# Kernel tuning notes

Hardware: AMD Instinct MI355X
Metric: run time of the kernel (lower is better)

Reference implementation:

```python
import jax, jax.numpy as jnp
import numpy as np

B, C, H, W = 32, 512, 32, 32


def setup_inputs() -> dict:
    key = jax.random.key(0)
    ks = jax.random.split(key, 7)
    c2 = C // 2
    s_in = (1.0 / C) ** 0.5   # torch Conv2d default init scale (kernel 1x1)
    s_c2 = (1.0 / c2) ** 0.5
    return {
        "x": jax.random.normal(ks[0], (B, C, H, W), jnp.float32),
        "Wk": jax.random.normal(ks[1], (c2, C), jnp.float32) * s_in,
        "bk": jax.random.normal(ks[2], (c2,), jnp.float32) * s_in,
        "Wv": jax.random.normal(ks[3], (c2, C), jnp.float32) * s_in,
        "bv": jax.random.normal(ks[4], (c2,), jnp.float32) * s_in,
        "Wo": jax.random.normal(ks[5], (C, c2), jnp.float32) * s_c2,
        "bo": jax.random.normal(ks[6], (C,), jnp.float32) * s_c2,
    }


def reference(x, Wk, bk, Wv, bv, Wo, bo):
    Bn, Cn, Hn, Wn = x.shape
    c2 = Cn // 2
    M = Hn * Wn
    # 1x1 convs as channel contractions
    k = jnp.einsum('oc,bchw->bohw', Wk, x) + bk[None, :, None, None]   # [B,c2,H,W]
    v = jnp.einsum('oc,bchw->bohw', Wv, x) + bv[None, :, None, None]   # [B,c2,H,W]
    # torch .reshape(B, M, c2) reinterprets memory (NOT a transpose) -> same in jnp
    v = v.reshape(Bn, M, c2)                                           # [B,M,c2]
    kf = k.reshape(Bn, c2, M)                                          # [B,c2,M]
    # cov_feature: k^T I_hat k with I_hat = (1/M)I - (1/M^2)11^T
    #            = (1/M) k^T k - (1/M^2) s s^T,  s = sum over channels
    gram = jnp.einsum('bcm,bcn->bmn', kf, kf) / M                      # [B,M,M]
    s = kf.sum(axis=1)                                                 # [B,M]
    cov = gram - (s[:, :, None] * s[:, None, :]) / (M * M)
    attn = jax.nn.softmax(cov * (c2 ** -0.5), axis=-1)                 # [B,M,M]
    out = jnp.einsum('bmn,bnc->bmc', attn, v)                          # [B,M,c2]
    # torch .view(B, c2, H, W) is also a raw memory reinterpretation
    out = out.reshape(Bn, c2, Hn, Wn)
    out = jnp.einsum('oc,bchw->bohw', Wo, out) + bo[None, :, None, None]
    return out + x
```

## Files before the change

### kernel.cpp

```cpp
#include <hip/hip_runtime.h>


typedef short bf8 __attribute__((ext_vector_type(8)));
typedef float f32x4 __attribute__((ext_vector_type(4)));

#define MFMA16(a, b, c) __builtin_amdgcn_mfma_f32_16x16x32_bf16((a), (b), (c), 0, 0, 0)

__device__ __forceinline__ short f2bf(float x) {
  unsigned u = __float_as_uint(x);
  u += 0x7fffu + ((u >> 16) & 1u);
  return (short)(u >> 16);
}

__device__ __forceinline__ void gll16(const short* g, void* l) {
  __builtin_amdgcn_global_load_lds(
      (const __attribute__((address_space(1))) unsigned int*)g,
      (__attribute__((address_space(3))) unsigned int*)l, 16, 0, 0);
}

__device__ __forceinline__ void lgkm0() {
  asm volatile("s_waitcnt lgkmcnt(0)" ::: "memory");
}
template <int N>
__device__ __forceinline__ void waitv() {
  static_assert(N == 0 || N == 4 || N == 8, "bad vmcnt");
  if constexpr (N == 0) asm volatile("s_waitcnt vmcnt(0)" ::: "memory");
  else if constexpr (N == 4) asm volatile("s_waitcnt vmcnt(4)" ::: "memory");
  else asm volatile("s_waitcnt vmcnt(8)" ::: "memory");
}
__device__ __forceinline__ void barrier_relaxed() {
  asm volatile("" ::: "memory");
  __builtin_amdgcn_s_barrier();
  asm volatile("" ::: "memory");
}

__device__ __forceinline__ void gemm_core(const short* __restrict__ A,
                                          const short* __restrict__ B,
                                          int ldA, int ldB, int ksteps,
                                          char* smem, f32x4 acc[4][4]) {
  const int tid = threadIdx.x;
  const int w = tid >> 6, l = tid & 63;
  const int q = l >> 4, i = l & 15;
  const int wm = w & 1, wn = w >> 1;
  const int srow = l >> 3;
  const int gcol = ((l & 7) ^ srow) * 8;
  f32x4 zz = {0.f, 0.f, 0.f, 0.f};
  #pragma unroll
  for (int mt = 0; mt < 4; ++mt)
    #pragma unroll
    for (int nt = 0; nt < 4; ++nt) acc[mt][nt] = zz;

  for (int ks = 0; ks < ksteps; ++ks) {
    __syncthreads();
    const short* Ak = A + ks * 64 + gcol;
    const short* Bk = B + ks * 64 + gcol;
    #pragma unroll
    for (int j = 0; j < 4; ++j) {
      int s = w * 4 + j;
      size_t row = (size_t)(s * 8 + srow);
      gll16(Ak + row * ldA, smem + s * 1024);
      gll16(Bk + row * ldB, smem + 16384 + s * 1024);
    }
    __syncthreads();
    #pragma unroll
    for (int kq = 0; kq < 2; ++kq) {
      int sw = ((kq * 4 + q) ^ (i & 7)) * 16;
      bf8 af[4], bq[4];
      #pragma unroll
      for (int mt = 0; mt < 4; ++mt)
        af[mt] = *(const bf8*)(smem + (wm * 64 + mt * 16 + i) * 128 + sw);
      #pragma unroll
      for (int nt = 0; nt < 4; ++nt)
        bq[nt] = *(const bf8*)(smem + 16384 + (wn * 64 + nt * 16 + i) * 128 + sw);
      #pragma unroll
      for (int mt = 0; mt < 4; ++mt)
        #pragma unroll
        for (int nt = 0; nt < 4; ++nt)
          acc[mt][nt] = MFMA16(af[mt], bq[nt], acc[mt][nt]);
    }
  }
}

__global__ __launch_bounds__(256) void p0_xpose(const float* __restrict__ x,
                                                short* __restrict__ xT) {
  __shared__ float lds[64][65];
  int cb = blockIdx.x, sb = blockIdx.y, b = blockIdx.z;
  int t = threadIdx.x;
  int c0 = cb * 64, sp0 = sb * 64;
  const float4* x4 = reinterpret_cast<const float4*>(x);
  #pragma unroll
  for (int j = 0; j < 4; ++j) {
    int lin = t + 256 * j;
    int cl = lin >> 4, s4 = lin & 15;
    float4 v = x4[(((size_t)b * 512 + c0 + cl) * 1024 + sp0 + s4 * 4) >> 2];
    lds[cl][s4 * 4 + 0] = v.x; lds[cl][s4 * 4 + 1] = v.y;
    lds[cl][s4 * 4 + 2] = v.z; lds[cl][s4 * 4 + 3] = v.w;
  }
  __syncthreads();
  int spl = t >> 2, cs = (t & 3) * 16;
  bf8 o0, o1;
  #pragma unroll
  for (int j = 0; j < 8; ++j) o0[j] = f2bf(lds[cs + j][spl]);
  #pragma unroll
  for (int j = 0; j < 8; ++j) o1[j] = f2bf(lds[cs + 8 + j][spl]);
  size_t base = ((size_t)b * 1024 + sp0 + spl) * 512 + c0 + cs;
  *reinterpret_cast<bf8*>(xT + base) = o0;
  *reinterpret_cast<bf8*>(xT + base + 8) = o1;
}

__global__ __launch_bounds__(256) void w0_weights(const float* __restrict__ Wk,
                                                  const float* __restrict__ Wv,
                                                  const float* __restrict__ Wo,
                                                  short* __restrict__ Wkv_bf,
                                                  short* __restrict__ Wo_bf) {
  int g = blockIdx.x * 256 + threadIdx.x;
  if (g < 262144) {
    int o = g >> 9, c = g & 511;
    float v = (o < 256) ? Wk[o * 512 + c] : Wv[(o - 256) * 512 + c];
    Wkv_bf[g] = f2bf(v);
  } else {
    int i2 = g - 262144;
    Wo_bf[i2] = f2bf(Wo[i2]);
  }
}

__global__ __launch_bounds__(256, 2) void k1_kv(const short* __restrict__ xT,
                                                const short* __restrict__ Wkv,
                                                const float* __restrict__ bk,
                                                const float* __restrict__ bv,
                                                short* __restrict__ kT,
                                                short* __restrict__ vT,
                                                float* __restrict__ s_part) {
  __shared__ __attribute__((aligned(16))) char smem[32768];
  f32x4 acc[4][4];
  int bm = blockIdx.x, bn = blockIdx.y;
  gemm_core(xT + (size_t)bm * 128 * 512, Wkv + (size_t)bn * 128 * 512,
            512, 512, 8, smem, acc);
  int tid = threadIdx.x;
  int w = tid >> 6, l = tid & 63, q = l >> 4, i = l & 15;
  int wm = w & 1, wn = w >> 1;
  int mbase = bm * 128 + wm * 64;
  int nbase = bn * 128 + wn * 64;
  if (bn < 2) {
    float rp[4][4];
    #pragma unroll
    for (int mt = 0; mt < 4; ++mt)
      #pragma unroll
      for (int r = 0; r < 4; ++r) rp[mt][r] = 0.f;
    #pragma unroll
    for (int mt = 0; mt < 4; ++mt)
      #pragma unroll
      for (int nt = 0; nt < 4; ++nt) {
        float bias = bk[nbase + nt * 16 + i];
        #pragma unroll
        for (int r = 0; r < 4; ++r) {
          float val = acc[mt][nt][r] + bias;
          int mg = mbase + mt * 16 + q * 4 + r;
          kT[(size_t)mg * 256 + nbase + nt * 16 + i] = f2bf(val);
          rp[mt][r] += val;
        }
      }
    #pragma unroll
    for (int mask = 1; mask <= 8; mask <<= 1)
      #pragma unroll
      for (int mt = 0; mt < 4; ++mt)
        #pragma unroll
        for (int r = 0; r < 4; ++r) rp[mt][r] += __shfl_xor(rp[mt][r], mask, 64);
    if (i == 0) {
      int pg = bn * 2 + wn;
      #pragma unroll
      for (int mt = 0; mt < 4; ++mt)
        #pragma unroll
        for (int r = 0; r < 4; ++r)
          s_part[pg * 32768 + mbase + mt * 16 + q * 4 + r] = rp[mt][r];
    }
  } else {
    #pragma unroll
    for (int mt = 0; mt < 4; ++mt)
      #pragma unroll
      for (int nt = 0; nt < 4; ++nt) {
        int o2 = nbase + nt * 16 + i - 256;
        float bias = bv[o2];
        #pragma unroll
        for (int r = 0; r < 4; ++r) {
          float val = acc[mt][nt][r] + bias;
          int mg = mbase + mt * 16 + q * 4 + r;
          int b = mg >> 10, sp = mg & 1023;
          vT[((size_t)b * 256 + (sp & 255)) * 1024 + 4 * o2 + (sp >> 8)] = f2bf(val);
        }
      }
  }
}

__global__ __launch_bounds__(256) void k1b_sum(const float* __restrict__ s_part,
                                               float* __restrict__ s_buf) {
  int t = blockIdx.x * 256 + threadIdx.x;
  s_buf[t] = s_part[t] + s_part[32768 + t] + s_part[65536 + t] + s_part[98304 + t];
}

__global__ __launch_bounds__(256, 2) void k2_fused(const short* __restrict__ kT,
                                                   const short* __restrict__ vT,
                                                   const float* __restrict__ s_buf,
                                                   short* __restrict__ OB) {
  __shared__ __attribute__((aligned(16))) char smem[81920];
  char* Apan = smem;
  char* Ppan = smem + 32768;
  char* Bst  = smem + 49152;

  const int id = blockIdx.x;
  const int xcd = id & 7, slot = id >> 3;
  const int b  = xcd * 4 + (slot >> 4);
  const int bm = slot & 15;

  const int tid = threadIdx.x;
  const int w = tid >> 6, l = tid & 63;
  const int q = l >> 4, i = l & 15;
  const int srow = l >> 3;
  const int gcol = ((l & 7) ^ srow) * 8;

  const short* kTb = kT + (size_t)b * 1024 * 256;
  const short* vTb = vT + (size_t)b * 256 * 1024;
  const float* sB = s_buf + b * 1024;

  char* slabA = Bst + w * 4096;
  char* slabB = Bst + 16384 + w * 4096;

  const float sc1 = 1.0f / 16384.0f;
  const float sc2 = 1.0f / 16777216.0f;

  float sm2[4][4];
  #pragma unroll
  for (int mt = 0; mt < 4; ++mt)
    #pragma unroll
    for (int r = 0; r < 4; ++r)
      sm2[mt][r] = sB[bm * 64 + mt * 16 + q * 4 + r] * sc2;
  float sn[8][2];
  #pragma unroll
  for (int c = 0; c < 8; ++c) {
    sn[c][0] = sB[c * 128 + w * 32 + i];
    sn[c][1] = sB[c * 128 + w * 32 + 16 + i];
  }

  auto stageS = [&](int c, int ks, char* sl) {
    const short* Bn = kTb + (size_t)c * 128 * 256 + ks * 64 + gcol;
    #pragma unroll
    for (int j = 0; j < 4; ++j)
      gll16(Bn + (size_t)(w * 32 + j * 8 + srow) * 256, sl + j * 1024);
  };
  auto stageV = [&](int c, int ks2, int h, char* sl) {
    const short* Vn = vTb + c * 128 + ks2 * 64 + gcol;
    #pragma unroll
    for (int j = 0; j < 4; ++j)
      gll16(Vn + (size_t)(w * 64 + h * 32 + j * 8 + srow) * 1024, sl + j * 1024);
  };

  {
    const short* Am = kTb + (size_t)bm * 64 * 256;
    #pragma unroll
    for (int ks = 0; ks < 4; ++ks)
      #pragma unroll
      for (int j2 = 0; j2 < 2; ++j2) {
        int s2 = w * 2 + j2;
        gll16(Am + (size_t)(s2 * 8 + srow) * 256 + ks * 64 + gcol,
              Apan + ks * 8192 + s2 * 1024);
      }
  }
  stageS(0, 0, slabA);
  stageS(0, 1, slabB);
  waitv<8>();
  barrier_relaxed();

  f32x4 zz = {0.f, 0.f, 0.f, 0.f};
  f32x4 acc_o[4][4];
  float rowsum[4][4];
  #pragma unroll
  for (int mt = 0; mt < 4; ++mt)
    #pragma unroll
    for (int ct = 0; ct < 4; ++ct) acc_o[mt][ct] = zz;
  #pragma unroll
  for (int mt = 0; mt < 4; ++mt)
    #pragma unroll
    for (int r = 0; r < 4; ++r) rowsum[mt][r] = 0.f;

  #pragma unroll
  for (int c = 0; c < 8; ++c) {
    f32x4 acc_s[4][2];
    #pragma unroll
    for (int mt = 0; mt < 4; ++mt)
      #pragma unroll
      for (int nt = 0; nt < 2; ++nt) acc_s[mt][nt] = zz;

    #pragma unroll
    for (int ks = 0; ks < 4; ++ks) {
      char* sl = (ks & 1) ? slabB : slabA;
      waitv<4>();
      #pragma unroll
      for (int kq = 0; kq < 2; ++kq) {
        int sw = ((kq * 4 + q) ^ (i & 7)) * 16;
        bf8 af[4], bq2[2];
        #pragma unroll
        for (int mt = 0; mt < 4; ++mt)
          af[mt] = *(const bf8*)(Apan + ks * 8192 + (mt * 16 + i) * 128 + sw);
        #pragma unroll
        for (int nt = 0; nt < 2; ++nt)
          bq2[nt] = *(const bf8*)(sl + (nt * 16 + i) * 128 + sw);
        __builtin_amdgcn_s_setprio(1);
        #pragma unroll
        for (int mt = 0; mt < 4; ++mt)
          #pragma unroll
          for (int nt = 0; nt < 2; ++nt)
            acc_s[mt][nt] = MFMA16(af[mt], bq2[nt], acc_s[mt][nt]);
        __builtin_amdgcn_s_setprio(0);
      }
      lgkm0();
      if (ks < 2) stageS(c, ks + 2, sl);
      else        stageV(c, 0, ks - 2, sl);
    }

    barrier_relaxed();
    #pragma unroll
    for (int nt = 0; nt < 2; ++nt) {
      float snv = sn[c][nt];
      int nl = w * 32 + nt * 16 + i;
      char* pbase = Ppan + (nl >> 6) * 8192 + (nl & 7) * 2;
      int gchunk = (nl >> 3) & 7;
      #pragma unroll
      for (int mt = 0; mt < 4; ++mt)
        #pragma unroll
        for (int r = 0; r < 4; ++r) {
          int ml = mt * 16 + q * 4 + r;
          float p = __expf(acc_s[mt][nt][r] * sc1 - sm2[mt][r] * snv);
          rowsum[mt][r] += p;
          *(short*)(pbase + ml * 128 + ((gchunk ^ (ml & 7)) * 16)) = f2bf(p);
        }
    }
    lgkm0();
    barrier_relaxed();

    #pragma unroll
    for (int pv = 0; pv < 4; ++pv) {
      char* sl = (pv & 1) ? slabB : slabA;
      const int ks2 = pv >> 1, h = pv & 1;
      if (c == 7 && pv == 3) waitv<0>(); else waitv<4>();
      #pragma unroll
      for (int kq = 0; kq < 2; ++kq) {
        int sw = ((kq * 4 + q) ^ (i & 7)) * 16;
        bf8 ap[4], bv2[2];
        #pragma unroll
        for (int mt = 0; mt < 4; ++mt)
          ap[mt] = *(const bf8*)(Ppan + ks2 * 8192 + (mt * 16 + i) * 128 + sw);
        #pragma unroll
        for (int u = 0; u < 2; ++u)
          bv2[u] = *(const bf8*)(sl + (u * 16 + i) * 128 + sw);
        __builtin_amdgcn_s_setprio(1);
        #pragma unroll
        for (int mt = 0; mt < 4; ++mt)
          #pragma unroll
          for (int u = 0; u < 2; ++u)
            acc_o[mt][h * 2 + u] = MFMA16(ap[mt], bv2[u], acc_o[mt][h * 2 + u]);
        __builtin_amdgcn_s_setprio(0);
      }
      lgkm0();
      if (pv < 2) stageV(c, 1, pv, sl);
      else if (c < 7) stageS(c + 1, pv - 2, sl);
    }
  }

  #pragma unroll
  for (int mask = 1; mask <= 8; mask <<= 1)
    #pragma unroll
    for (int mt = 0; mt < 4; ++mt)
      #pragma unroll
      for (int r = 0; r < 4; ++r) rowsum[mt][r] += __shfl_xor(rowsum[mt][r], mask, 64);
  __syncthreads();
  float* rs = (float*)Ppan;
  if (i == 0) {
    #pragma unroll
    for (int mt = 0; mt < 4; ++mt)
      #pragma unroll
      for (int r = 0; r < 4; ++r)
        rs[w * 64 + mt * 16 + q * 4 + r] = rowsum[mt][r];
  }
  __syncthreads();
  float rinv[4][4];
  #pragma unroll
  for (int mt = 0; mt < 4; ++mt)
    #pragma unroll
    for (int r = 0; r < 4; ++r) {
      int m = mt * 16 + q * 4 + r;
      rinv[mt][r] = 1.0f / (rs[m] + rs[64 + m] + rs[128 + m] + rs[192 + m]);
    }
  short* ob = (short*)(Bst + w * 8192);
  #pragma unroll
  for (int mt = 0; mt < 4; ++mt)
    #pragma unroll
    for (int ct = 0; ct < 4; ++ct)
      #pragma unroll
      for (int r = 0; r < 4; ++r)
        ob[(r * 64 + ct * 16 + i) * 16 + mt * 4 + q] =
            f2bf(acc_o[mt][ct][r] * rinv[mt][r]);
  short* obg = OB + (size_t)b * 1024 * 256;
  #pragma unroll
  for (int jj = 0; jj < 8; ++jj) {
    int lr = jj * 32 + (l >> 1), ch = l & 1;
    bf8 vv = *(const bf8*)(ob + lr * 16 + ch * 8);
    int rr = lr >> 6, cc = lr & 63;
    *(bf8*)(obg + ((size_t)(rr * 256 + w * 64 + cc)) * 256 + bm * 16 + ch * 8) = vv;
  }
}

__global__ __launch_bounds__(256, 2) void k3_out(const short* __restrict__ Wo_bf,
                                                 const short* __restrict__ OB,
                                                 const float* __restrict__ bo,
                                                 const float* __restrict__ x,
                                                 float* __restrict__ out) {
  __shared__ __attribute__((aligned(16))) char smem[32768];
  f32x4 acc[4][4];
  int bm = blockIdx.x, bn = blockIdx.y, b = blockIdx.z;
  gemm_core(Wo_bf + (size_t)bm * 128 * 256,
            OB + ((size_t)b * 1024 + bn * 128) * 256, 256, 256, 4, smem, acc);
  int tid = threadIdx.x;
  int w = tid >> 6, l = tid & 63, q = l >> 4, i = l & 15;
  int wm = w & 1, wn = w >> 1;
  int oloc = bm * 128 + wm * 64, sploc = bn * 128 + wn * 64;
  #pragma unroll
  for (int mt = 0; mt < 4; ++mt)
    #pragma unroll
    for (int r = 0; r < 4; ++r) {
      int o = oloc + mt * 16 + q * 4 + r;
      float bias = bo[o];
      #pragma unroll
      for (int nt = 0; nt < 4; ++nt) {
        int sp = sploc + nt * 16 + i;
        size_t idx = ((size_t)b * 512 + o) * 1024 + sp;
        out[idx] = acc[mt][nt][r] + bias + x[idx];
      }
    }
}

extern "C" void kernel_launch(void* const* d_in, const int* in_sizes, int n_in,
                              void* d_out, int out_size, void* d_ws, size_t ws_size,
                              hipStream_t stream) {
  (void)in_sizes; (void)n_in; (void)out_size; (void)ws_size;
  const float* x  = (const float*)d_in[0];
  const float* Wk = (const float*)d_in[1];
  const float* bk = (const float*)d_in[2];
  const float* Wv = (const float*)d_in[3];
  const float* bv = (const float*)d_in[4];
  const float* Wo = (const float*)d_in[5];
  const float* bo = (const float*)d_in[6];
  float* out = (float*)d_out;
  char* ws = (char*)d_ws;

  short* xT     = (short*)(ws);
  short* OB     = (short*)(ws);
  short* kTb    = (short*)(ws + 33554432);
  short* vTb    = (short*)(ws + 50331648);
  short* Wkv_bf = (short*)(ws + 67108864);
  short* Wo_bf  = (short*)(ws + 67633152);
  float* s_part = (float*)(ws + 67895296);
  float* s_buf  = (float*)(ws + 68419584);

  p0_xpose<<<dim3(8, 16, 32), 256, 0, stream>>>(x, xT);
  w0_weights<<<1536, 256, 0, stream>>>(Wk, Wv, Wo, Wkv_bf, Wo_bf);
  k1_kv<<<dim3(256, 4), 256, 0, stream>>>(xT, Wkv_bf, bk, bv, kTb, vTb, s_part);
  k1b_sum<<<128, 256, 0, stream>>>(s_part, s_buf);
  k2_fused<<<dim3(512), 256, 0, stream>>>(kTb, vTb, s_buf, OB);
  k3_out<<<dim3(4, 8, 32), 256, 0, stream>>>(Wo_bf, OB, bo, x, out);
}
```

Baseline: 233.0 us.

## Fuse s-sum into attention kernel and hold half the query panel in registers

Removes the separate k1b_sum launch: each k2_fused block reduces the four s_part partials for its batch into a new LDS buffer and reads its row and column sums from there. The first two k-steps of the query (A) panel are loaded into registers once and reused for all eight key chunks, so only half of the A panel stays in LDS, cutting LDS use from 80 KB to 68 KB. This reduces LDS read traffic and one kernel launch, at the cost of many more VGPRs per thread, redundant reduction work across the 16 blocks per batch, and a full vmcnt(0) wait in the prologue.

New measurement: 263.2 us. 13.0% more time.

```diff
diff --git a/kernel.cpp b/kernel.cpp
--- a/kernel.cpp
+++ b/kernel.cpp
@@ -32,6 +32,32 @@
   asm volatile("" ::: "memory");
   __builtin_amdgcn_s_barrier();
   asm volatile("" ::: "memory");
+}
+
+__device__ __forceinline__ void s_kq(const char* base, int sw,
+                                     bf8 A0, bf8 A1, bf8 A2, bf8 A3,
+                                     f32x4 (&acc)[4][2]) {
+  bf8 b0 = *(const bf8*)(base + sw);
+  bf8 b1 = *(const bf8*)(base + 2048 + sw);
+  __builtin_amdgcn_s_setprio(1);
+  acc[0][0] = MFMA16(A0, b0, acc[0][0]);
+  acc[0][1] = MFMA16(A0, b1, acc[0][1]);
+  acc[1][0] = MFMA16(A1, b0, acc[1][0]);
+  acc[1][1] = MFMA16(A1, b1, acc[1][1]);
+  acc[2][0] = MFMA16(A2, b0, acc[2][0]);
+  acc[2][1] = MFMA16(A2, b1, acc[2][1]);
+  acc[3][0] = MFMA16(A3, b0, acc[3][0]);
+  acc[3][1] = MFMA16(A3, b1, acc[3][1]);
+  __builtin_amdgcn_s_setprio(0);
+}
+
+__device__ __forceinline__ void s_kq_lds(const char* base, const char* ap,
+                                         int sw, f32x4 (&acc)[4][2]) {
+  bf8 A0 = *(const bf8*)(ap + sw);
+  bf8 A1 = *(const bf8*)(ap + 2048 + sw);
+  bf8 A2 = *(const bf8*)(ap + 4096 + sw);
+  bf8 A3 = *(const bf8*)(ap + 6144 + sw);
+  s_kq(base, sw, A0, A1, A2, A3, acc);
 }
 
 __device__ __forceinline__ void gemm_core(const short* __restrict__ A,
@@ -192,20 +218,15 @@
   }
 }
 
-__global__ __launch_bounds__(256) void k1b_sum(const float* __restrict__ s_part,
-                                               float* __restrict__ s_buf) {
-  int t = blockIdx.x * 256 + threadIdx.x;
-  s_buf[t] = s_part[t] + s_part[32768 + t] + s_part[65536 + t] + s_part[98304 + t];
-}
-
 __global__ __launch_bounds__(256, 2) void k2_fused(const short* __restrict__ kT,
                                                    const short* __restrict__ vT,
-                                                   const float* __restrict__ s_buf,
+                                                   const float* __restrict__ s_part,
                                                    short* __restrict__ OB) {
-  __shared__ __attribute__((aligned(16))) char smem[81920];
+  __shared__ __attribute__((aligned(16))) char smem[69632];
   char* Apan = smem;
-  char* Ppan = smem + 32768;
-  char* Bst  = smem + 49152;
+  char* Ppan = smem + 16384;
+  char* Bst  = smem + 32768;
+  float* sLDS = (float*)(smem + 65536);
 
   const int id = blockIdx.x;
   const int xcd = id & 7, slot = id >> 3;
@@ -220,7 +241,6 @@
 
   const short* kTb = kT + (size_t)b * 1024 * 256;
   const short* vTb = vT + (size_t)b * 256 * 1024;
-  const float* sB = s_buf + b * 1024;
 
   char* slabA = Bst + w * 4096;
   char* slabB = Bst + 16384 + w * 4096;
@@ -228,18 +248,75 @@
   const float sc1 = 1.0f / 16384.0f;
   const float sc2 = 1.0f / 16777216.0f;
 
+  {
+    const short* Am = kTb + (size_t)bm * 64 * 256;
+    #pragma unroll
+    for (int ks = 0; ks < 2; ++ks)
+      #pragma unroll
+      for (int j2 = 0; j2 < 2; ++j2) {
+        int s2 = w * 2 + j2;
+        gll16(Am + (size_t)(s2 * 8 + srow) * 256 + ks * 64 + gcol,
+              Bst + ks * 8192 + s2 * 1024);
+      }
+    #pragma unroll
+    for (int ks = 2; ks < 4; ++ks)
+      #pragma unroll
+      for (int j2 = 0; j2 < 2; ++j2) {
+        int s2 = w * 2 + j2;
+        gll16(Am + (size_t)(s2 * 8 + srow) * 256 + ks * 64 + gcol,
+              Apan + (ks - 2) * 8192 + s2 * 1024);
+      }
+  }
+
+  const int mglob = b * 1024;
+  {
+    const float4* p0 = (const float4*)(s_part + mglob) + tid;
+    const float4* p1 = (const float4*)(s_part + 32768 + mglob) + tid;
+    const float4* p2 = (const float4*)(s_part + 65536 + mglob) + tid;
+    const float4* p3 = (const float4*)(s_part + 98304 + mglob) + tid;
+    float4 v0 = *p0, v1 = *p1, v2 = *p2, v3 = *p3;
+    float4 s;
+    s.x = v0.x + v1.x + v2.x + v3.x;
+    s.y = v0.y + v1.y + v2.y + v3.y;
+    s.z = v0.z + v1.z + v2.z + v3.z;
+    s.w = v0.w + v1.w + v2.w + v3.w;
+    ((float4*)sLDS)[tid] = s;
+  }
+
+  waitv<0>();
+  lgkm0();
+  barrier_relaxed();
+
+  const int sw0 = (q ^ (i & 7)) * 16;
+  const int sw1 = ((4 + q) ^ (i & 7)) * 16;
+  const char* fb0 = Bst + i * 128;
+  const char* fb1 = Bst + 8192 + i * 128;
+  bf8 a000 = *(const bf8*)(fb0 + sw0);
+  bf8 a001 = *(const bf8*)(fb0 + 2048 + sw0);
+  bf8 a002 = *(const bf8*)(fb0 + 4096 + sw0);
+  bf8 a003 = *(const bf8*)(fb0 + 6144 + sw0);
+  bf8 a010 = *(const bf8*)(fb0 + sw1);
+  bf8 a011 = *(const bf8*)(fb0 + 2048 + sw1);
+  bf8 a012 = *(const bf8*)(fb0 + 4096 + sw1);
+  bf8 a013 = *(const bf8*)(fb0 + 6144 + sw1);
+  bf8 a100 = *(const bf8*)(fb1 + sw0);
+  bf8 a101 = *(const bf8*)(fb1 + 2048 + sw0);
+  bf8 a102 = *(const bf8*)(fb1 + 4096 + sw0);
+  bf8 a103 = *(const bf8*)(fb1 + 6144 + sw0);
+  bf8 a110 = *(const bf8*)(fb1 + sw1);
+  bf8 a111 = *(const bf8*)(fb1 + 2048 + sw1);
+  bf8 a112 = *(const bf8*)(fb1 + 4096 + sw1);
+  bf8 a113 = *(const bf8*)(fb1 + 6144 + sw1);
+
   float sm2[4][4];
   #pragma unroll
   for (int mt = 0; mt < 4; ++mt)
     #pragma unroll
     for (int r = 0; r < 4; ++r)
-      sm2[mt][r] = sB[bm * 64 + mt * 16 + q * 4 + r] * sc2;
-  float sn[8][2];
-  #pragma unroll
-  for (int c = 0; c < 8; ++c) {
-    sn[c][0] = sB[c * 128 + w * 32 + i];
-    sn[c][1] = sB[c * 128 + w * 32 + 16 + i];
-  }
+      sm2[mt][r] = sLDS[bm * 64 + mt * 16 + q * 4 + r] * sc2;
+
+  lgkm0();
+  barrier_relaxed();
 
   auto stageS = [&](int c, int ks, char* sl) {
     const short* Bn = kTb + (size_t)c * 128 * 256 + ks * 64 + gcol;
@@ -254,21 +331,8 @@
       gll16(Vn + (size_t)(w * 64 + h * 32 + j * 8 + srow) * 1024, sl + j * 1024);
   };
 
-  {
-    const short* Am = kTb + (size_t)bm * 64 * 256;
-    #pragma unroll
-    for (int ks = 0; ks < 4; ++ks)
-      #pragma unroll
-      for (int j2 = 0; j2 < 2; ++j2) {
-        int s2 = w * 2 + j2;
-        gll16(Am + (size_t)(s2 * 8 + srow) * 256 + ks * 64 + gcol,
-              Apan + ks * 8192 + s2 * 1024);
-      }
-  }
   stageS(0, 0, slabA);
   stageS(0, 1, slabB);
-  waitv<8>();
-  barrier_relaxed();
 
   f32x4 zz = {0.f, 0.f, 0.f, 0.f};
   f32x4 acc_o[4][4];
@@ -282,6 +346,11 @@
     #pragma unroll
     for (int r = 0; r < 4; ++r) rowsum[mt][r] = 0.f;
 
+  const char* sA = slabA + i * 128;
+  const char* sB = slabB + i * 128;
+  const char* ap0 = Apan + i * 128;
+  const char* ap1 = Apan + 8192 + i * 128;
+
   #pragma unroll
   for (int c = 0; c < 8; ++c) {
     f32x4 acc_s[4][2];
@@ -290,37 +359,36 @@
       #pragma unroll
       for (int nt = 0; nt < 2; ++nt) acc_s[mt][nt] = zz;
 
-    #pragma unroll
-    for (int ks = 0; ks < 4; ++ks) {
-      char* sl = (ks & 1) ? slabB : slabA;
-      waitv<4>();
-      #pragma unroll
-      for (int kq = 0; kq < 2; ++kq) {
-        int sw = ((kq * 4 + q) ^ (i & 7)) * 16;
-        bf8 af[4], bq2[2];
-        #pragma unroll
-        for (int mt = 0; mt < 4; ++mt)
-          af[mt] = *(const bf8*)(Apan + ks * 8192 + (mt * 16 + i) * 128 + sw);
-        #pragma unroll
-        for (int nt = 0; nt < 2; ++nt)
-          bq2[nt] = *(const bf8*)(sl + (nt * 16 + i) * 128 + sw);
-        __builtin_amdgcn_s_setprio(1);
-        #pragma unroll
-        for (int mt = 0; mt < 4; ++mt)
-          #pragma unroll
-          for (int nt = 0; nt < 2; ++nt)
-            acc_s[mt][nt] = MFMA16(af[mt], bq2[nt], acc_s[mt][nt]);
-        __builtin_amdgcn_s_setprio(0);
-      }
-      lgkm0();
-      if (ks < 2) stageS(c, ks + 2, sl);
-      else        stageV(c, 0, ks - 2, sl);
-    }
+    waitv<4>();
+    s_kq(sA, sw0, a000, a001, a002, a003, acc_s);
+    s_kq(sA, sw1, a010, a011, a012, a013, acc_s);
+    lgkm0();
+    stageS(c, 2, slabA);
+
+    waitv<4>();
+    s_kq(sB, sw0, a100, a101, a102, a103, acc_s);
+    s_kq(sB, sw1, a110, a111, a112, a113, acc_s);
+    lgkm0();
+    stageS(c, 3, slabB);
+
+    waitv<4>();
+    s_kq_lds(sA, ap0, sw0, acc_s);
+    s_kq_lds(sA, ap0, sw1, acc_s);
+    lgkm0();
+    stageV(c, 0, 0, slabA);
+
+    waitv<4>();
+    s_kq_lds(sB, ap1, sw0, acc_s);
+    s_kq_lds(sB, ap1, sw1, acc_s);
+    lgkm0();
+    stageV(c, 0, 1, slabB);
 
     barrier_relaxed();
+    float snv0 = sLDS[c * 128 + w * 32 + i];
+    float snv1 = sLDS[c * 128 + w * 32 + 16 + i];
     #pragma unroll
     for (int nt = 0; nt < 2; ++nt) {
-      float snv = sn[c][nt];
+      float snv = nt ? snv1 : snv0;
       int nl = w * 32 + nt * 16 + i;
       char* pbase = Ppan + (nl >> 6) * 8192 + (nl & 7) * 2;
       int gchunk = (nl >> 3) & 7;
@@ -459,12 +527,10 @@
   short* Wkv_bf = (short*)(ws + 67108864);
   short* Wo_bf  = (short*)(ws + 67633152);
   float* s_part = (float*)(ws + 67895296);
-  float* s_buf  = (float*)(ws + 68419584);
 
   p0_xpose<<<dim3(8, 16, 32), 256, 0, stream>>>(x, xT);
   w0_weights<<<1536, 256, 0, stream>>>(Wk, Wv, Wo, Wkv_bf, Wo_bf);
   k1_kv<<<dim3(256, 4), 256, 0, stream>>>(xT, Wkv_bf, bk, bv, kTb, vTb, s_part);
-  k1b_sum<<<128, 256, 0, stream>>>(s_part, s_buf);
-  k2_fused<<<dim3(512), 256, 0, stream>>>(kTb, vTb, s_buf, OB);
+  k2_fused<<<dim3(512), 256, 0, stream>>>(kTb, vTb, s_part, OB);
   k3_out<<<dim3(4, 8, 32), 256, 0, stream>>>(Wo_bf, OB, bo, x, out);
 }
```
